# Optimization experiments

Measured on AMD Instinct MI355X. Metric: run time of the kernel, lower is better.

The kernel has to match this reference:

```python
import jax, jax.numpy as jnp
import numpy as np


def _params_to_tokens(params):
    # (batch, 2k) -> (batch, k, 2) : chunk into freqs/amps then stack
    freqs, amps = jnp.split(params, 2, axis=-1)
    return jnp.stack((freqs, amps), axis=-1)


def setup_inputs() -> dict:
    key = jax.random.key(0)
    k1, k2 = jax.random.split(key)
    predicted = jax.random.normal(k1, (64, 4096), dtype=jnp.float32)
    target = jax.random.normal(k2, (64, 4096), dtype=jnp.float32)
    return {"predicted": predicted, "target": target}


def reference(predicted, target):
    p = _params_to_tokens(predicted)   # (b, k, 2)
    t = _params_to_tokens(target)      # (b, k, 2)
    # Euclidean cdist via gram-matrix identity (avoids (b,k,k,2) broadcast temp)
    p2 = jnp.sum(p * p, axis=-1)       # (b, k)
    t2 = jnp.sum(t * t, axis=-1)       # (b, k)
    gram = jnp.einsum('bid,bjd->bij', p, t)  # (b, k, k)
    sq = p2[:, :, None] + t2[:, None, :] - 2.0 * gram
    costs = jnp.sqrt(jnp.maximum(sq, 0.0))   # (b, k, k)
    min1 = jnp.mean(jnp.min(costs, axis=1), axis=-1)  # min over predicted dim
    min2 = jnp.mean(jnp.min(costs, axis=2), axis=-1)  # min over target dim
    return jnp.mean(min1 + min2)
```

## Files before the change

kernel.cpp:

```cpp
#include <hip/hip_runtime.h>


typedef _Float16 f16;
typedef _Float16 f16x8 __attribute__((ext_vector_type(8)));
typedef float f32x16 __attribute__((ext_vector_type(16)));

constexpr int K = 2048;
constexpr int BLOCK = 512;
constexpr int NBAND = 8;
constexpr int BAND = 256;
constexpr int NJT = K / 32;
constexpr unsigned INF_U = 0x7F800000u;

#define MFMA16 __builtin_amdgcn_mfma_f32_32x32x16_f16

#define DPP_MIN(m, ctrl)                                                   \
  {                                                                        \
    int _i = __builtin_bit_cast(int, m);                                   \
    int _r = __builtin_amdgcn_update_dpp(_i, _i, (ctrl), 0xF, 0xF, false); \
    m = fminf(m, __builtin_bit_cast(float, _r));                           \
  }

__device__ __forceinline__ unsigned pk(f16 lo, f16 hi) {
  unsigned a = (unsigned)__builtin_bit_cast(unsigned short, lo);
  unsigned b = (unsigned)__builtin_bit_cast(unsigned short, hi);
  return a | (b << 16);
}
__device__ __forceinline__ unsigned split2(float v) {
  const f16 h = (f16)v;
  const f16 l = (f16)(v - (float)h);
  return pk(h, l);
}
__device__ __forceinline__ float min3p(float a, float b, float c) {
  return fminf(fminf(a, b), c);
}

__global__ __launch_bounds__(BLOCK, 4) void chamfer_mfma(
    const float* __restrict__ pred, const float* __restrict__ targ,
    float* __restrict__ out, float* __restrict__ ws) {
  const int iband = blockIdx.x;
  const int b = blockIdx.y;
  const int tid = threadIdx.x;
  const int lane = tid & 63;
  const int w = tid >> 6;
  const int r = lane & 31;
  const bool lo_half = (lane < 32);

  __shared__ uint4 BrecP[K + 1];
  __shared__ uint4 ArecP[2 * BAND];
  __shared__ unsigned colmin_u[K];
  __shared__ unsigned rowmin_u[BAND];

  const float* tb = targ + (size_t)b * (2 * K);
  const float* pb = pred + (size_t)b * (2 * K);

  #pragma unroll
  for (int k = 0; k < K / BLOCK; ++k) {
    const int j = tid + k * BLOCK;
    const float x = tb[j], y = tb[K + j];
    const unsigned wx = split2(x);
    const unsigned wy = split2(y);
    const unsigned wt = split2(fmaf(x, x, y * y));
    BrecP[j] = make_uint4(wx,
                          (wx & 0xffffu) | (wy << 16),
                          (wy >> 16) | (wy << 16),
                          wt);
    colmin_u[j] = INF_U;
  }
  if (tid == 0) BrecP[K] = make_uint4(0x3C003C00u, 0u, 0u, 0u);
  if (tid < BAND) {
    const int i = iband * BAND + tid;
    const float x = pb[i], y = pb[K + i];
    const unsigned wu = split2(-2.0f * x);
    const unsigned ww = split2(-2.0f * y);
    const unsigned wp = split2(fmaf(x, x, y * y));
    ArecP[tid] = make_uint4((wu & 0xffffu) | (wu << 16),
                            (wu >> 16) | (ww << 16),
                            ww,
                            0x3C003C00u);
    ArecP[BAND + tid] = make_uint4(wp, 0u, 0u, 0u);
    rowmin_u[tid] = INF_U;
  }
  __syncthreads();

  const f32x16 zero = {};

  const f16x8 af = __builtin_bit_cast(
      f16x8, ArecP[(lo_half ? 0 : BAND) + w * 32 + r]);

  f32x16 rowacc;
  #pragma unroll
  for (int q = 0; q < 16; ++q) rowacc[q] = 3.4e38f;

  int bidx = lo_half ? r : (int)K;
  const int bstep = lo_half ? 32 : 0;

  auto compute = [&](const uint4& q4, int jt) {
    const f32x16 d = MFMA16(af, __builtin_bit_cast(f16x8, q4), zero, 0, 0, 0);
    #pragma unroll
    for (int q = 0; q < 16; ++q) rowacc[q] = fminf(rowacc[q], d[q]);
    const float a0 = min3p(d[0], d[1], d[2]);
    const float a1 = min3p(d[3], d[4], d[5]);
    const float a2 = min3p(d[6], d[7], d[8]);
    const float a3 = min3p(d[9], d[10], d[11]);
    const float a4 = min3p(d[12], d[13], d[14]);
    float cm = fminf(min3p(a0, a1, a2), min3p(a3, a4, d[15]));
    cm = fmaxf(cm, 0.0f);
    atomicMin(&colmin_u[jt * 32 + r], __float_as_uint(cm));
  };

  uint4 cq = BrecP[bidx];
  bidx += bstep;
  #pragma unroll 1
  for (int jt = 0; jt < NJT - 1; ++jt) {
    const uint4 nq = BrecP[bidx];
    bidx += bstep;
    compute(cq, jt);
    cq = nq;
  }
  compute(cq, NJT - 1);

  #pragma unroll
  for (int q = 0; q < 16; ++q) {
    float m = rowacc[q];
    DPP_MIN(m, 0x111); DPP_MIN(m, 0x112); DPP_MIN(m, 0x114);
    DPP_MIN(m, 0x118); DPP_MIN(m, 0x142);
    rowacc[q] = m;
  }
  if (lane == 31 || lane == 63) {
    const int rb = w * 32 + ((lane >> 5) << 4);
    #pragma unroll
    for (int q = 0; q < 16; ++q) {
      const float cm = fmaxf(rowacc[q], 0.0f);
      atomicMin(&rowmin_u[rb + q], __float_as_uint(cm));
    }
  }
  __syncthreads();

  if (w == 0) {
    const uint4 v = *(const uint4*)&rowmin_u[lane * 4];
    float s = sqrtf(__uint_as_float(v.x)) + sqrtf(__uint_as_float(v.y)) +
              sqrtf(__uint_as_float(v.z)) + sqrtf(__uint_as_float(v.w));
    #pragma unroll
    for (int off = 32; off; off >>= 1) s += __shfl_xor(s, off, 64);
    if (lane == 0) atomicAdd(out, s * (1.0f / 131072.0f));
  } else if (w >= 4) {
    float* wrow = ws + (size_t)(b * NBAND + iband) * K;
    const int t8 = (tid - 256) * 8;
    *(uint4*)&wrow[t8]     = *(const uint4*)&colmin_u[t8];
    *(uint4*)&wrow[t8 + 4] = *(const uint4*)&colmin_u[t8 + 4];
  }
}

__global__ __launch_bounds__(256, 4) void chamfer_pass2(
    const float* __restrict__ ws, float* __restrict__ out) {
  const int b = blockIdx.x >> 2;
  const int qt = blockIdx.x & 3;
  const int tid = threadIdx.x;
  __shared__ float wsum[4];
  const float* wrow = ws + (size_t)b * NBAND * K;
  float s = 0.0f;
  #pragma unroll
  for (int k = 0; k < 2; ++k) {
    const int j = qt * 512 + k * 256 + tid;
    float m = wrow[j];
    #pragma unroll
    for (int band = 1; band < NBAND; ++band) m = fminf(m, wrow[band * K + j]);
    s += sqrtf(m);
  }
  #pragma unroll
  for (int off = 32; off; off >>= 1) s += __shfl_down(s, off, 64);
  const int lane = tid & 63, w = tid >> 6;
  if (lane == 0) wsum[w] = s;
  __syncthreads();
  if (tid == 0)
    atomicAdd(out, (wsum[0] + wsum[1] + wsum[2] + wsum[3]) * (1.0f / 131072.0f));
}

extern "C" void kernel_launch(void* const* d_in, const int* in_sizes, int n_in,
                              void* d_out, int out_size, void* d_ws, size_t ws_size,
                              hipStream_t stream) {
  const float* pred = (const float*)d_in[0];
  const float* targ = (const float*)d_in[1];
  float* out = (float*)d_out;
  float* ws = (float*)d_ws;

  dim3 g1(NBAND, 64);
  chamfer_mfma<<<g1, dim3(BLOCK), 0, stream>>>(pred, targ, out, ws);
  chamfer_pass2<<<dim3(256), dim3(256), 0, stream>>>(ws, out);
}
```

Before: 97.91 us.

## Pre-pack target records in a separate kernel and stream B operands from global memory

```diff
diff --git a/kernel.cpp b/kernel.cpp
--- a/kernel.cpp
+++ b/kernel.cpp
@@ -11,15 +11,9 @@
 constexpr int BAND = 256;
 constexpr int NJT = K / 32;
 constexpr unsigned INF_U = 0x7F800000u;
+constexpr size_t COL_WS = (size_t)64 * NBAND * K;
 
 #define MFMA16 __builtin_amdgcn_mfma_f32_32x32x16_f16
-
-#define DPP_MIN(m, ctrl)                                                   \
-  {                                                                        \
-    int _i = __builtin_bit_cast(int, m);                                   \
-    int _r = __builtin_amdgcn_update_dpp(_i, _i, (ctrl), 0xF, 0xF, false); \
-    m = fminf(m, __builtin_bit_cast(float, _r));                           \
-  }
 
 __device__ __forceinline__ unsigned pk(f16 lo, f16 hi) {
   unsigned a = (unsigned)__builtin_bit_cast(unsigned short, lo);
@@ -35,9 +29,33 @@
   return fminf(fminf(a, b), c);
 }
 
+__global__ __launch_bounds__(512, 4) void chamfer_pack(
+    const float* __restrict__ targ, float* __restrict__ ws) {
+  const int b = blockIdx.x;
+  const int tid = threadIdx.x;
+  uint4* bp = (uint4*)(ws + COL_WS) + (size_t)b * K;
+  const float* tb = targ + (size_t)b * (2 * K);
+  #pragma unroll
+  for (int k = 0; k < K / 512; ++k) {
+    const int j = tid + k * 512;
+    const float x = tb[j], y = tb[K + j];
+    const unsigned wx = split2(x);
+    const unsigned wy = split2(y);
+    const unsigned wt = split2(fmaf(x, x, y * y));
+    bp[j] = make_uint4(wx,
+                       (wx & 0xffffu) | (wy << 16),
+                       (wy >> 16) | (wy << 16),
+                       wt);
+  }
+  if (b == 0 && tid == 0) {
+    ((uint4*)(ws + COL_WS))[(size_t)64 * K] =
+        make_uint4(0x3C003C00u, 0u, 0u, 0u);
+  }
+}
+
 __global__ __launch_bounds__(BLOCK, 4) void chamfer_mfma(
-    const float* __restrict__ pred, const float* __restrict__ targ,
-    float* __restrict__ out, float* __restrict__ ws) {
+    const float* __restrict__ pred, float* __restrict__ out,
+    float* __restrict__ ws) {
   const int iband = blockIdx.x;
   const int b = blockIdx.y;
   const int tid = threadIdx.x;
@@ -46,28 +64,13 @@
   const int r = lane & 31;
   const bool lo_half = (lane < 32);
 
-  __shared__ uint4 BrecP[K + 1];
   __shared__ uint4 ArecP[2 * BAND];
   __shared__ unsigned colmin_u[K];
-  __shared__ unsigned rowmin_u[BAND];
+  __shared__ float wsum[8];
 
-  const float* tb = targ + (size_t)b * (2 * K);
   const float* pb = pred + (size_t)b * (2 * K);
 
-  #pragma unroll
-  for (int k = 0; k < K / BLOCK; ++k) {
-    const int j = tid + k * BLOCK;
-    const float x = tb[j], y = tb[K + j];
-    const unsigned wx = split2(x);
-    const unsigned wy = split2(y);
-    const unsigned wt = split2(fmaf(x, x, y * y));
-    BrecP[j] = make_uint4(wx,
-                          (wx & 0xffffu) | (wy << 16),
-                          (wy >> 16) | (wy << 16),
-                          wt);
-    colmin_u[j] = INF_U;
-  }
-  if (tid == 0) BrecP[K] = make_uint4(0x3C003C00u, 0u, 0u, 0u);
+  *(uint4*)&colmin_u[tid * 4] = make_uint4(INF_U, INF_U, INF_U, INF_U);
   if (tid < BAND) {
     const int i = iband * BAND + tid;
     const float x = pb[i], y = pb[K + i];
@@ -79,7 +82,6 @@
                             ww,
                             0x3C003C00u);
     ArecP[BAND + tid] = make_uint4(wp, 0u, 0u, 0u);
-    rowmin_u[tid] = INF_U;
   }
   __syncthreads();
 
@@ -92,7 +94,8 @@
   #pragma unroll
   for (int q = 0; q < 16; ++q) rowacc[q] = 3.4e38f;
 
-  int bidx = lo_half ? r : (int)K;
+  const uint4* bq = (const uint4*)(ws + COL_WS);
+  size_t bidx = lo_half ? ((size_t)b * K + r) : ((size_t)64 * K);
   const int bstep = lo_half ? 32 : 0;
 
   auto compute = [&](const uint4& q4, int jt) {
@@ -109,47 +112,43 @@
     atomicMin(&colmin_u[jt * 32 + r], __float_as_uint(cm));
   };
 
-  uint4 cq = BrecP[bidx];
-  bidx += bstep;
+  uint4 c0 = bq[bidx];
+  uint4 c1 = bq[bidx + bstep];
+  bidx += 2 * (size_t)bstep;
   #pragma unroll 1
-  for (int jt = 0; jt < NJT - 1; ++jt) {
-    const uint4 nq = BrecP[bidx];
-    bidx += bstep;
-    compute(cq, jt);
-    cq = nq;
+  for (int jt = 0; jt < NJT - 2; jt += 2) {
+    const uint4 n0 = bq[bidx];
+    const uint4 n1 = bq[bidx + bstep];
+    bidx += 2 * (size_t)bstep;
+    compute(c0, jt);
+    compute(c1, jt + 1);
+    c0 = n0;
+    c1 = n1;
   }
-  compute(cq, NJT - 1);
+  compute(c0, NJT - 2);
+  compute(c1, NJT - 1);
 
   #pragma unroll
-  for (int q = 0; q < 16; ++q) {
-    float m = rowacc[q];
-    DPP_MIN(m, 0x111); DPP_MIN(m, 0x112); DPP_MIN(m, 0x114);
-    DPP_MIN(m, 0x118); DPP_MIN(m, 0x142);
-    rowacc[q] = m;
+  for (int m = 1; m <= 16; m <<= 1) {
+    #pragma unroll
+    for (int q = 0; q < 16; ++q)
+      rowacc[q] = fminf(rowacc[q], __shfl_xor(rowacc[q], m, 64));
   }
-  if (lane == 31 || lane == 63) {
-    const int rb = w * 32 + ((lane >> 5) << 4);
+  float s = 0.0f;
+  #pragma unroll
+  for (int q = 0; q < 16; ++q) s += sqrtf(fmaxf(rowacc[q], 0.0f));
+  s += __shfl_xor(s, 32, 64);
+  if (lane == 0) wsum[w] = s;
+  __syncthreads();
+  if (tid == 0) {
+    float t = 0.0f;
     #pragma unroll
-    for (int q = 0; q < 16; ++q) {
-      const float cm = fmaxf(rowacc[q], 0.0f);
-      atomicMin(&rowmin_u[rb + q], __float_as_uint(cm));
-    }
+    for (int i = 0; i < 8; ++i) t += wsum[i];
+    atomicAdd(out, t * (1.0f / 131072.0f));
   }
-  __syncthreads();
-
-  if (w == 0) {
-    const uint4 v = *(const uint4*)&rowmin_u[lane * 4];
-    float s = sqrtf(__uint_as_float(v.x)) + sqrtf(__uint_as_float(v.y)) +
-              sqrtf(__uint_as_float(v.z)) + sqrtf(__uint_as_float(v.w));
-    #pragma unroll
-    for (int off = 32; off; off >>= 1) s += __shfl_xor(s, off, 64);
-    if (lane == 0) atomicAdd(out, s * (1.0f / 131072.0f));
-  } else if (w >= 4) {
-    float* wrow = ws + (size_t)(b * NBAND + iband) * K;
-    const int t8 = (tid - 256) * 8;
-    *(uint4*)&wrow[t8]     = *(const uint4*)&colmin_u[t8];
-    *(uint4*)&wrow[t8 + 4] = *(const uint4*)&colmin_u[t8 + 4];
-  }
+  float* wrow = ws + (size_t)(b * NBAND + iband) * K;
+  const int t4 = tid * 4;
+  *(uint4*)&wrow[t4] = *(const uint4*)&colmin_u[t4];
 }
 
 __global__ __launch_bounds__(256, 4) void chamfer_pass2(
@@ -185,7 +184,8 @@
   float* out = (float*)d_out;
   float* ws = (float*)d_ws;
 
+  chamfer_pack<<<dim3(64), dim3(512), 0, stream>>>(targ, ws);
   dim3 g1(NBAND, 64);
-  chamfer_mfma<<<g1, dim3(BLOCK), 0, stream>>>(pred, targ, out, ws);
+  chamfer_mfma<<<g1, dim3(BLOCK), 0, stream>>>(pred, out, ws);
   chamfer_pass2<<<dim3(256), dim3(256), 0, stream>>>(ws, out);
 }
```

New measurement: 87.90 us. 10.2% less time.
